# Performance work log

Measured on AMD Instinct MI355X. Metric: run time of the kernel, lower is better.

The kernel has to match this reference:

```python
import jax, jax.numpy as jnp
import numpy as np

B, N, L, D_IN, D = 32, 2048, 32768, 4, 64


def setup_inputs() -> dict:
    key = jax.random.key(0)
    ks = jax.random.split(key, 10)
    s = 0.05  # modest init scale for params
    return {
        "pred_node": jax.random.normal(ks[0], (B, N, D_IN), jnp.float32),
        "line_param": jax.random.normal(ks[1], (B, L, 4), jnp.float32),
        "W_embed": jax.random.normal(ks[2], (D_IN, D), jnp.float32) * s,
        "b_embed": jnp.zeros((D,), jnp.float32),
        "W1": jax.random.normal(ks[3], (2 * D, D), jnp.float32) * s,
        "b1": jnp.zeros((D,), jnp.float32),
        "W2": jax.random.normal(ks[4], (D, 4), jnp.float32) * s,
        "b2": jnp.zeros((4,), jnp.float32),
        "edge_src": jax.random.randint(ks[5], (B, L), 0, N, jnp.int32),
        "edge_dst": jax.random.randint(ks[6], (B, L), 0, N, jnp.int32),
    }


def reference(pred_node, line_param, W_embed, b_embed, W1, b1, W2, b2,
              edge_src, edge_dst):
    # node_feat_to_line_feat: Linear(4 -> d_model) over all nodes at once
    node_feat = jnp.einsum("bni,id->bnd", pred_node, W_embed) + b_embed  # (B,N,D)

    # Batched gather of node-feature pairs per edge (replaces Python loops)
    fi = jnp.take_along_axis(node_feat, edge_src[..., None].astype(jnp.int32), axis=1)  # (B,L,D)
    fj = jnp.take_along_axis(node_feat, edge_dst[..., None].astype(jnp.int32), axis=1)  # (B,L,D)
    combined = jnp.concatenate([fi, fj], axis=-1)  # (B,L,2D)

    # line_pred_head: Linear(2D->D) -> ReLU -> Dropout(eval: identity) -> Linear(D->4)
    h = jax.nn.relu(jnp.einsum("ble,ed->bld", combined, W1) + b1)
    line_pred = jnp.einsum("bld,do->blo", h, W2) + b2  # (B,L,4)

    # Cols 0,1 copied from line_param; cols 2,3 from the prediction head
    out = jnp.concatenate([line_param[..., :2], line_pred[..., 2:4]], axis=-1)
    return out
```

## Files before the change

### kernel.cpp

```cpp
#include <hip/hip_runtime.h>
#include <hip/hip_fp16.h>
#include <stdint.h>

#define B_ 32
#define N_ 2048
#define L_ 32768


static __device__ __forceinline__ __half2 pkrn(float a, float b) {
    return __float22half2_rn(make_float2(a, b));
}

static __device__ __forceinline__ __half2 pkmax(__half2 a, __half2 b) {
    __half2 r;
    asm("v_pk_max_f16 %0, %1, %2" : "=v"(r) : "v"(a), "v"(b));
    return r;
}

static __device__ __forceinline__ __half2 bits_h2(float x) {
    union { float f; __half2 h; } u;
    u.f = x;
    return u.h;
}

__global__ __launch_bounds__(256, 8) void fused_kernel(
    const float4* __restrict__ pred_node,
    const float* __restrict__ W_embed, const float* __restrict__ b_embed,
    const float* __restrict__ W1, const float* __restrict__ b1,
    const float* __restrict__ W2, const float* __restrict__ b2,
    const int* __restrict__ esrc, const int* __restrict__ edst,
    const float2* __restrict__ lp2,
    float4* __restrict__ out) {
    __shared__ __align__(16) __half2 swh[64 * 12];

    const int tid = threadIdx.x;
    const int bid = blockIdx.x;
    const int x = bid & 7;
    const int i = bid >> 3;
    const int b = x + 8 * (i >> 6);
    const int j = i & 63;
    const int ebase = b * L_ + j * 512 + tid;

    int s0 = esrc[ebase], s1 = esrc[ebase + 256];
    int t0 = edst[ebase], t1 = edst[ebase + 256];

    {
        const int f = tid & 63;
        const int g = tid >> 6;
        float acc_t = 0.f, acc_b = 0.f, acc_bias = 0.f;
#pragma unroll 8
        for (int k = 0; k < 64; ++k) {
            float wt = W1[k * 64 + f];
            float wb = W1[(64 + k) * 64 + f];
            float we = W_embed[g * 64 + k];
            acc_t = fmaf(we, wt, acc_t);
            acc_b = fmaf(we, wb, acc_b);
            if (g == 0) acc_bias = fmaf(b_embed[k], wt + wb, acc_bias);
        }
        swh[f * 12 + g] = pkrn(acc_t, acc_t);
        swh[f * 12 + 4 + g] = pkrn(acc_b, acc_b);
        if (g == 0) {
            float bv = acc_bias + b1[f];
            swh[f * 12 + 8] = pkrn(bv, bv);
        } else if (g == 1) {
            float c2 = W2[f * 4 + 2];
            swh[f * 12 + 9] = pkrn(c2, c2);
        } else if (g == 2) {
            float c3 = W2[f * 4 + 3];
            swh[f * 12 + 10] = pkrn(c3, c3);
        } else {
            swh[f * 12 + 11] = pkrn(0.f, 0.f);
        }
    }

    __syncthreads();

    const float4* pnb = pred_node + b * N_;
    float4 vs0 = pnb[s0];
    float4 vs1 = pnb[s1];
    float4 vt0 = pnb[t0];
    float4 vt1 = pnb[t1];

    __half2 px0 = pkrn(vs0.x, vs1.x);
    __half2 px1 = pkrn(vs0.y, vs1.y);
    __half2 px2 = pkrn(vs0.z, vs1.z);
    __half2 px3 = pkrn(vs0.w, vs1.w);
    __half2 px4 = pkrn(vt0.x, vt1.x);
    __half2 px5 = pkrn(vt0.y, vt1.y);
    __half2 px6 = pkrn(vt0.z, vt1.z);
    __half2 px7 = pkrn(vt0.w, vt1.w);

    const __half2 zero = pkrn(0.f, 0.f);
    __half2 acc2 = zero, acc3 = zero;

#pragma unroll 4
    for (int f = 0; f < 64; ++f) {
        const float4* wv = reinterpret_cast<const float4*>(swh) + f * 3;
        float4 q0 = wv[0], q1 = wv[1], q2 = wv[2];
        __half2 h = bits_h2(q2.x);
        h = __hfma2(px0, bits_h2(q0.x), h);
        h = __hfma2(px1, bits_h2(q0.y), h);
        h = __hfma2(px2, bits_h2(q0.z), h);
        h = __hfma2(px3, bits_h2(q0.w), h);
        h = __hfma2(px4, bits_h2(q1.x), h);
        h = __hfma2(px5, bits_h2(q1.y), h);
        h = __hfma2(px6, bits_h2(q1.z), h);
        h = __hfma2(px7, bits_h2(q1.w), h);
        h = pkmax(h, zero);
        acc2 = __hfma2(h, bits_h2(q2.y), acc2);
        acc3 = __hfma2(h, bits_h2(q2.z), acc3);
    }

    float bias2 = b2[2], bias3 = b2[3];
    float2 lp0 = lp2[(size_t)ebase * 2];
    float2 lp1 = lp2[(size_t)(ebase + 256) * 2];
    out[ebase] = make_float4(lp0.x, lp0.y,
                             bias2 + __low2float(acc2),
                             bias3 + __low2float(acc3));
    out[ebase + 256] = make_float4(lp1.x, lp1.y,
                                   bias2 + __high2float(acc2),
                                   bias3 + __high2float(acc3));
}

extern "C" void kernel_launch(void* const* d_in, const int* in_sizes, int n_in,
                              void* d_out, int out_size, void* d_ws, size_t ws_size,
                              hipStream_t stream) {
    const float* pred_node = (const float*)d_in[0];
    const float* line_param = (const float*)d_in[1];
    const float* W_embed = (const float*)d_in[2];
    const float* b_embed = (const float*)d_in[3];
    const float* W1 = (const float*)d_in[4];
    const float* b1 = (const float*)d_in[5];
    const float* W2 = (const float*)d_in[6];
    const float* b2 = (const float*)d_in[7];
    const int* esrc = (const int*)d_in[8];
    const int* edst = (const int*)d_in[9];
    float* out = (float*)d_out;

    fused_kernel<<<2048, 256, 0, stream>>>((const float4*)pred_node,
                                           W_embed, b_embed, W1, b1, W2, b2,
                                           esrc, edst,
                                           (const float2*)line_param,
                                           (float4*)out);
}
```

Measured before the change: 116.8 us.

## Serve folded weight table through scalar loads from a global workspace

The per-block folded weight table (W_embed·W1, bias, W2 columns) is no longer kept in LDS. It is written to a per-block slice of the global workspace by the first 64 threads, each of which now computes all four embed rows. The inner loop then fetches each 48-byte record with s_load_dwordx4 into SGPRs, which takes the LDS reads and VGPR pressure out of the hot loop. The line_param loads are also issued earlier so their latency overlaps the table setup. The risks: each iteration ends with a full lgkmcnt wait, which serialises the scalar fetches. Scalar-cache coherence with the vector stores depends on the barrier and on L2. The prologue is also more serial because only 64 threads build the table, and the change needs a 4 MB workspace.

```diff
diff --git a/kernel.cpp b/kernel.cpp
--- a/kernel.cpp
+++ b/kernel.cpp
@@ -6,6 +6,8 @@
 #define N_ 2048
 #define L_ 32768
 
+
+typedef unsigned int u32x4 __attribute__((ext_vector_type(4)));
 
 static __device__ __forceinline__ __half2 pkrn(float a, float b) {
     return __float22half2_rn(make_float2(a, b));
@@ -17,10 +19,12 @@
     return r;
 }
 
-static __device__ __forceinline__ __half2 bits_h2(float x) {
-    union { float f; __half2 h; } u;
-    u.f = x;
-    return u.h;
+static __device__ __forceinline__ unsigned int h2u(__half2 h) {
+    union { __half2 h; unsigned int u; } c; c.h = h; return c.u;
+}
+
+static __device__ __forceinline__ __half2 u2h(unsigned int u) {
+    union { unsigned int u; __half2 h; } c; c.u = u; return c.h;
 }
 
 __global__ __launch_bounds__(256, 8) void fused_kernel(
@@ -30,9 +34,8 @@
     const float* __restrict__ W2, const float* __restrict__ b2,
     const int* __restrict__ esrc, const int* __restrict__ edst,
     const float2* __restrict__ lp2,
+    unsigned int* __restrict__ wstab,
     float4* __restrict__ out) {
-    __shared__ __align__(16) __half2 swh[64 * 12];
-
     const int tid = threadIdx.x;
     const int bid = blockIdx.x;
     const int x = bid & 7;
@@ -43,37 +46,55 @@
 
     int s0 = esrc[ebase], s1 = esrc[ebase + 256];
     int t0 = edst[ebase], t1 = edst[ebase + 256];
+    float2 lp0 = lp2[(size_t)ebase * 2];
+    float2 lp1 = lp2[(size_t)(ebase + 256) * 2];
 
-    {
-        const int f = tid & 63;
-        const int g = tid >> 6;
-        float acc_t = 0.f, acc_b = 0.f, acc_bias = 0.f;
+    unsigned int* tbl = wstab + (size_t)bid * 512;
+
+    if (tid < 64) {
+        const int f = tid;
+        float at0 = 0.f, at1 = 0.f, at2 = 0.f, at3 = 0.f;
+        float ab0 = 0.f, ab1 = 0.f, ab2 = 0.f, ab3 = 0.f;
+        float bia = 0.f;
 #pragma unroll 8
         for (int k = 0; k < 64; ++k) {
             float wt = W1[k * 64 + f];
             float wb = W1[(64 + k) * 64 + f];
-            float we = W_embed[g * 64 + k];
-            acc_t = fmaf(we, wt, acc_t);
-            acc_b = fmaf(we, wb, acc_b);
-            if (g == 0) acc_bias = fmaf(b_embed[k], wt + wb, acc_bias);
+            float e0 = W_embed[k];
+            float e1 = W_embed[64 + k];
+            float e2 = W_embed[128 + k];
+            float e3 = W_embed[192 + k];
+            at0 = fmaf(e0, wt, at0);
+            at1 = fmaf(e1, wt, at1);
+            at2 = fmaf(e2, wt, at2);
+            at3 = fmaf(e3, wt, at3);
+            ab0 = fmaf(e0, wb, ab0);
+            ab1 = fmaf(e1, wb, ab1);
+            ab2 = fmaf(e2, wb, ab2);
+            ab3 = fmaf(e3, wb, ab3);
+            bia = fmaf(b_embed[k], wt + wb, bia);
         }
-        swh[f * 12 + g] = pkrn(acc_t, acc_t);
-        swh[f * 12 + 4 + g] = pkrn(acc_b, acc_b);
-        if (g == 0) {
-            float bv = acc_bias + b1[f];
-            swh[f * 12 + 8] = pkrn(bv, bv);
-        } else if (g == 1) {
-            float c2 = W2[f * 4 + 2];
-            swh[f * 12 + 9] = pkrn(c2, c2);
-        } else if (g == 2) {
-            float c3 = W2[f * 4 + 3];
-            swh[f * 12 + 10] = pkrn(c3, c3);
-        } else {
-            swh[f * 12 + 11] = pkrn(0.f, 0.f);
-        }
+        bia += b1[f];
+        float c2 = W2[f * 4 + 2], c3 = W2[f * 4 + 3];
+
+        u32x4 q0, q1, q2;
+        q0.x = h2u(pkrn(at0, at0));
+        q0.y = h2u(pkrn(at1, at1));
+        q0.z = h2u(pkrn(at2, at2));
+        q0.w = h2u(pkrn(at3, at3));
+        q1.x = h2u(pkrn(ab0, ab0));
+        q1.y = h2u(pkrn(ab1, ab1));
+        q1.z = h2u(pkrn(ab2, ab2));
+        q1.w = h2u(pkrn(ab3, ab3));
+        q2.x = h2u(pkrn(bia, bia));
+        q2.y = h2u(pkrn(c2, c2));
+        q2.z = h2u(pkrn(c3, c3));
+        q2.w = 0u;
+        u32x4* rec = reinterpret_cast<u32x4*>(tbl + f * 12);
+        rec[0] = q0;
+        rec[1] = q1;
+        rec[2] = q2;
     }
-
-    __syncthreads();
 
     const float4* pnb = pred_node + b * N_;
     float4 vs0 = pnb[s0];
@@ -90,30 +111,39 @@
     __half2 px6 = pkrn(vt0.z, vt1.z);
     __half2 px7 = pkrn(vt0.w, vt1.w);
 
-    const __half2 zero = pkrn(0.f, 0.f);
+    __syncthreads();
+
+    const __half2 zero = u2h(0u);
     __half2 acc2 = zero, acc3 = zero;
+    const uint64_t tbase = (uint64_t)(uintptr_t)tbl;
 
-#pragma unroll 4
+#pragma unroll 2
     for (int f = 0; f < 64; ++f) {
-        const float4* wv = reinterpret_cast<const float4*>(swh) + f * 3;
-        float4 q0 = wv[0], q1 = wv[1], q2 = wv[2];
-        __half2 h = bits_h2(q2.x);
-        h = __hfma2(px0, bits_h2(q0.x), h);
-        h = __hfma2(px1, bits_h2(q0.y), h);
-        h = __hfma2(px2, bits_h2(q0.z), h);
-        h = __hfma2(px3, bits_h2(q0.w), h);
-        h = __hfma2(px4, bits_h2(q1.x), h);
-        h = __hfma2(px5, bits_h2(q1.y), h);
-        h = __hfma2(px6, bits_h2(q1.z), h);
-        h = __hfma2(px7, bits_h2(q1.w), h);
+        u32x4 q0, q1, q2;
+        uint64_t addr = tbase + (uint64_t)(f * 48);
+        asm volatile(
+            "s_load_dwordx4 %0, %3, 0x0\n\t"
+            "s_load_dwordx4 %1, %3, 0x10\n\t"
+            "s_load_dwordx4 %2, %3, 0x20\n\t"
+            "s_waitcnt lgkmcnt(0)"
+            : "=&s"(q0), "=&s"(q1), "=&s"(q2)
+            : "s"(addr)
+            : "memory");
+        __half2 h = u2h(q2.x);
+        h = __hfma2(px0, u2h(q0.x), h);
+        h = __hfma2(px1, u2h(q0.y), h);
+        h = __hfma2(px2, u2h(q0.z), h);
+        h = __hfma2(px3, u2h(q0.w), h);
+        h = __hfma2(px4, u2h(q1.x), h);
+        h = __hfma2(px5, u2h(q1.y), h);
+        h = __hfma2(px6, u2h(q1.z), h);
+        h = __hfma2(px7, u2h(q1.w), h);
         h = pkmax(h, zero);
-        acc2 = __hfma2(h, bits_h2(q2.y), acc2);
-        acc3 = __hfma2(h, bits_h2(q2.z), acc3);
+        acc2 = __hfma2(h, u2h(q2.y), acc2);
+        acc3 = __hfma2(h, u2h(q2.z), acc3);
     }
 
     float bias2 = b2[2], bias3 = b2[3];
-    float2 lp0 = lp2[(size_t)ebase * 2];
-    float2 lp1 = lp2[(size_t)(ebase + 256) * 2];
     out[ebase] = make_float4(lp0.x, lp0.y,
                              bias2 + __low2float(acc2),
                              bias3 + __low2float(acc3));
@@ -141,5 +171,6 @@
                                            W_embed, b_embed, W1, b1, W2, b2,
                                            esrc, edst,
                                            (const float2*)line_param,
+                                           (unsigned int*)d_ws,
                                            (float4*)out);
 }
```

Result: slower. 130.5 us (+11.8%).
